# Kernel tuning notes

Measured on AMD Instinct MI355X. Metric: run time of the kernel, lower is better.

The kernel has to match this reference:

```python
import jax, jax.numpy as jnp
import numpy as np

EPS_NORM = 1e-8   # matches torch F.normalize default-ish eps used in cosine_dist
CLAMP_MIN = 1e-12
CLAMP_MAX = 1e12

def setup_inputs() -> dict:
    key = jax.random.key(0)
    k1, k2, k3 = jax.random.split(key, 3)
    N, D, C = 262144, 256, 64
    ref_emb = jax.random.normal(k1, (N, D), dtype=jnp.float32)
    ref_label = jax.random.randint(k2, (N,), 0, C)
    centers = jax.random.normal(k3, (C, D), dtype=jnp.float32)
    return {"ref_emb": ref_emb, "ref_label": ref_label, "centers": centers}

def reference(ref_emb, ref_label, centers):
    # center[i] = centers[ref_label[i]]  -> [N, D] gather
    center = centers[ref_label]
    # diag of pairwise cosine-distance matrix == row-wise cosine distance
    # cos_dist_i = 1 - <x_i, c_i> / (||x_i|| * ||c_i||)
    dot = jnp.sum(ref_emb * center, axis=-1)                     # [N]
    nx = jnp.sqrt(jnp.sum(ref_emb * ref_emb, axis=-1))           # [N]
    nc = jnp.sqrt(jnp.sum(center * center, axis=-1))             # [N]
    cos_sim = dot / jnp.maximum(nx * nc, EPS_NORM)
    cos_diag = 1.0 - cos_sim
    return jnp.mean(jnp.clip(cos_diag, CLAMP_MIN, CLAMP_MAX), axis=-1)
```

## Files before the change

### kernel.cpp

```cpp
#include <hip/hip_runtime.h>
#include <math.h>

constexpr int N = 262144;
constexpr int D = 256;
constexpr int C = 64;
constexpr float CLAMP_MIN = 1e-12f;
constexpr float CLAMP_MAX = 1e12f;

constexpr int BLOCKS = 2048;
constexpr int NWAVES = BLOCKS * 4;
constexpr int GPW    = (N / 4) / NWAVES;

__global__ __launch_bounds__(64) void center_normalize_kernel(
        const float* __restrict__ centers, float* __restrict__ cn) {
    const int c = blockIdx.x;
    const int lane = threadIdx.x;
    float4 v = reinterpret_cast<const float4*>(centers + c * D)[lane];
    float s = v.x * v.x + v.y * v.y + v.z * v.z + v.w * v.w;
    #pragma unroll
    for (int off = 32; off >= 1; off >>= 1)
        s += __shfl_xor(s, off, 64);
    const float inv = rsqrtf(fmaxf(s, 1e-24f));
    float4 o = make_float4(v.x * inv, v.y * inv, v.z * inv, v.w * inv);
    reinterpret_cast<float4*>(cn + c * D)[lane] = o;
}

__global__ __launch_bounds__(256) void inner_cos_kernel(
        const float* __restrict__ emb,
        const int*   __restrict__ label,
        const float* __restrict__ cnormed,
        float* __restrict__ partials) {
    const int lane = threadIdx.x & 63;
    const int wave = threadIdx.x >> 6;
    const int sub  = lane & 15;
    const int quad = lane >> 4;
    const int gwave = (blockIdx.x << 2) | wave;

    int mylab = 0;
    if (lane < 32) {
        const int k = lane >> 2, q = lane & 3;
        mylab = label[4 * gwave + k * (4 * NWAVES) + q];
    }

    const float4* xbase = reinterpret_cast<const float4*>(emb);
    const float4* cbase = reinterpret_cast<const float4*>(cnormed);

    float lsum = 0.0f;
    float4 x[4], c[4];

    {
        const int lab  = __shfl(mylab, quad);
        const int row0 = 4 * gwave + quad;
        const float4* xr = xbase + (size_t)row0 * (D / 4);
        const float4* cr = cbase + (size_t)lab  * (D / 4);
        #pragma unroll
        for (int j = 0; j < 4; ++j) { x[j] = xr[(j << 4) + sub]; c[j] = cr[(j << 4) + sub]; }
    }

    #pragma unroll
    for (int k = 0; k < GPW; ++k) {
        float4 xn[4], cn[4];
        if (k + 1 < GPW) {
            const int labn = __shfl(mylab, ((k + 1) << 2) + quad);
            const int rown = 4 * gwave + (k + 1) * (4 * NWAVES) + quad;
            const float4* xr = xbase + (size_t)rown * (D / 4);
            const float4* cr = cbase + (size_t)labn * (D / 4);
            #pragma unroll
            for (int j = 0; j < 4; ++j) { xn[j] = xr[(j << 4) + sub]; cn[j] = cr[(j << 4) + sub]; }
        }

        float dot = 0.0f, nx2 = 0.0f;
        #pragma unroll
        for (int j = 0; j < 4; ++j) {
            dot = fmaf(x[j].x, c[j].x, dot); dot = fmaf(x[j].y, c[j].y, dot);
            dot = fmaf(x[j].z, c[j].z, dot); dot = fmaf(x[j].w, c[j].w, dot);
            nx2 = fmaf(x[j].x, x[j].x, nx2); nx2 = fmaf(x[j].y, x[j].y, nx2);
            nx2 = fmaf(x[j].z, x[j].z, nx2); nx2 = fmaf(x[j].w, x[j].w, nx2);
        }
        #pragma unroll
        for (int off = 8; off >= 1; off >>= 1) {
            dot += __shfl_xor(dot, off, 64);
            nx2 += __shfl_xor(nx2, off, 64);
        }
        float cd = 1.0f - dot * rsqrtf(fmaxf(nx2, 1e-24f));
        cd = fminf(fmaxf(cd, CLAMP_MIN), CLAMP_MAX);
        lsum += cd;

        if (k + 1 < GPW) {
            #pragma unroll
            for (int j = 0; j < 4; ++j) { x[j] = xn[j]; c[j] = cn[j]; }
        }
    }

    lsum += __shfl_xor(lsum, 16, 64);
    lsum += __shfl_xor(lsum, 32, 64);

    __shared__ float ssum[4];
    if (lane == 0) ssum[wave] = lsum;
    __syncthreads();
    if (threadIdx.x == 0)
        partials[blockIdx.x] = (ssum[0] + ssum[1]) + (ssum[2] + ssum[3]);
}

__global__ __launch_bounds__(256) void finalize_kernel(
        const float* __restrict__ partials, float* __restrict__ out) {
    float s = 0.0f;
    #pragma unroll
    for (int i = 0; i < BLOCKS / 256; ++i)
        s += partials[threadIdx.x + (i << 8)];
    #pragma unroll
    for (int off = 32; off >= 1; off >>= 1)
        s += __shfl_xor(s, off, 64);
    __shared__ float ss[4];
    if ((threadIdx.x & 63) == 0) ss[threadIdx.x >> 6] = s;
    __syncthreads();
    if (threadIdx.x == 0)
        out[0] = ((ss[0] + ss[1]) + (ss[2] + ss[3])) * (1.0f / (float)N);
}

extern "C" void kernel_launch(void* const* d_in, const int* in_sizes, int n_in,
                              void* d_out, int out_size, void* d_ws, size_t ws_size,
                              hipStream_t stream) {
    const float* emb     = (const float*)d_in[0];
    const int*   label   = (const int*)d_in[1];
    const float* centers = (const float*)d_in[2];
    float* out      = (float*)d_out;
    float* cnormed  = (float*)d_ws;
    float* partials = (float*)d_ws + C * D;

    center_normalize_kernel<<<C, 64, 0, stream>>>(centers, cnormed);
    inner_cos_kernel<<<BLOCKS, 256, 0, stream>>>(emb, label, cnormed, partials);
    finalize_kernel<<<1, 256, 0, stream>>>(partials, out);
}
```

Before: 357.4 us.

## Stage normalized centers in LDS and use nontemporal embedding loads

Each 1024-thread block copies the whole normalized center table into shared memory, and center rows are then read from LDS instead of being gathered from global memory. Embedding rows are loaded with nontemporal hints, and the grid changes to 512 blocks of 16 waves. This is meant to remove redundant global and L2 traffic for center gathers and keep the streamed embeddings from polluting the cache. The cost is a 64 KB per-block LDS fill, a block-wide barrier before compute, and lower occupancy.

```diff
diff --git a/kernel.cpp b/kernel.cpp
--- a/kernel.cpp
+++ b/kernel.cpp
@@ -7,9 +7,12 @@
 constexpr float CLAMP_MIN = 1e-12f;
 constexpr float CLAMP_MAX = 1e12f;
 
-constexpr int BLOCKS = 2048;
-constexpr int NWAVES = BLOCKS * 4;
-constexpr int GPW    = (N / 4) / NWAVES;
+constexpr int BLOCKS  = 512;
+constexpr int WPB     = 16;
+constexpr int NWAVES  = BLOCKS * WPB;
+constexpr int GPW     = (N / 4) / NWAVES;
+
+typedef float fvec4 __attribute__((ext_vector_type(4)));
 
 __global__ __launch_bounds__(64) void center_normalize_kernel(
         const float* __restrict__ centers, float* __restrict__ cn) {
@@ -25,16 +28,26 @@
     reinterpret_cast<float4*>(cn + c * D)[lane] = o;
 }
 
-__global__ __launch_bounds__(256) void inner_cos_kernel(
+__global__ __launch_bounds__(1024) void inner_cos_kernel(
         const float* __restrict__ emb,
         const int*   __restrict__ label,
         const float* __restrict__ cnormed,
         float* __restrict__ partials) {
+    __shared__ float4 ctab[C * D / 4];
+    __shared__ float  ssum[WPB];
+
+    {
+        const float4* src = reinterpret_cast<const float4*>(cnormed);
+        #pragma unroll
+        for (int i = 0; i < (C * D / 4) / 1024; ++i)
+            ctab[threadIdx.x + i * 1024] = src[threadIdx.x + i * 1024];
+    }
+
     const int lane = threadIdx.x & 63;
     const int wave = threadIdx.x >> 6;
     const int sub  = lane & 15;
     const int quad = lane >> 4;
-    const int gwave = (blockIdx.x << 2) | wave;
+    const int gwave = blockIdx.x * WPB + wave;
 
     int mylab = 0;
     if (lane < 32) {
@@ -42,38 +55,47 @@
         mylab = label[4 * gwave + k * (4 * NWAVES) + q];
     }
 
-    const float4* xbase = reinterpret_cast<const float4*>(emb);
-    const float4* cbase = reinterpret_cast<const float4*>(cnormed);
+    __syncthreads();
+
+    const fvec4* xbase = reinterpret_cast<const fvec4*>(emb);
 
     float lsum = 0.0f;
-    float4 x[4], c[4];
+    fvec4 x[4];
 
     {
-        const int lab  = __shfl(mylab, quad);
-        const int row0 = 4 * gwave + quad;
-        const float4* xr = xbase + (size_t)row0 * (D / 4);
-        const float4* cr = cbase + (size_t)lab  * (D / 4);
+        const fvec4* xr = xbase + (size_t)(4 * gwave + quad) * (D / 4);
         #pragma unroll
-        for (int j = 0; j < 4; ++j) { x[j] = xr[(j << 4) + sub]; c[j] = cr[(j << 4) + sub]; }
+        for (int j = 0; j < 4; ++j)
+            x[j] = __builtin_nontemporal_load(xr + (j << 4) + sub);
     }
 
     #pragma unroll
     for (int k = 0; k < GPW; ++k) {
-        float4 xn[4], cn[4];
+        fvec4 xn[4];
         if (k + 1 < GPW) {
-            const int labn = __shfl(mylab, ((k + 1) << 2) + quad);
             const int rown = 4 * gwave + (k + 1) * (4 * NWAVES) + quad;
-            const float4* xr = xbase + (size_t)rown * (D / 4);
-            const float4* cr = cbase + (size_t)labn * (D / 4);
+            const fvec4* xr = xbase + (size_t)rown * (D / 4);
             #pragma unroll
-            for (int j = 0; j < 4; ++j) { xn[j] = xr[(j << 4) + sub]; cn[j] = cr[(j << 4) + sub]; }
+            for (int j = 0; j < 4; ++j)
+                xn[j] = __builtin_nontemporal_load(xr + (j << 4) + sub);
         }
 
+        const int lab = __shfl(mylab, (k << 2) + quad);
+        const float4* crow = ctab + lab * (D / 4);
+        float4 c0 = crow[sub +  0], c1 = crow[sub + 16];
+        float4 c2 = crow[sub + 32], c3 = crow[sub + 48];
+
         float dot = 0.0f, nx2 = 0.0f;
+        dot = fmaf(x[0].x, c0.x, dot); dot = fmaf(x[0].y, c0.y, dot);
+        dot = fmaf(x[0].z, c0.z, dot); dot = fmaf(x[0].w, c0.w, dot);
+        dot = fmaf(x[1].x, c1.x, dot); dot = fmaf(x[1].y, c1.y, dot);
+        dot = fmaf(x[1].z, c1.z, dot); dot = fmaf(x[1].w, c1.w, dot);
+        dot = fmaf(x[2].x, c2.x, dot); dot = fmaf(x[2].y, c2.y, dot);
+        dot = fmaf(x[2].z, c2.z, dot); dot = fmaf(x[2].w, c2.w, dot);
+        dot = fmaf(x[3].x, c3.x, dot); dot = fmaf(x[3].y, c3.y, dot);
+        dot = fmaf(x[3].z, c3.z, dot); dot = fmaf(x[3].w, c3.w, dot);
         #pragma unroll
         for (int j = 0; j < 4; ++j) {
-            dot = fmaf(x[j].x, c[j].x, dot); dot = fmaf(x[j].y, c[j].y, dot);
-            dot = fmaf(x[j].z, c[j].z, dot); dot = fmaf(x[j].w, c[j].w, dot);
             nx2 = fmaf(x[j].x, x[j].x, nx2); nx2 = fmaf(x[j].y, x[j].y, nx2);
             nx2 = fmaf(x[j].z, x[j].z, nx2); nx2 = fmaf(x[j].w, x[j].w, nx2);
         }
@@ -88,18 +110,21 @@
 
         if (k + 1 < GPW) {
             #pragma unroll
-            for (int j = 0; j < 4; ++j) { x[j] = xn[j]; c[j] = cn[j]; }
+            for (int j = 0; j < 4; ++j) x[j] = xn[j];
         }
     }
 
     lsum += __shfl_xor(lsum, 16, 64);
     lsum += __shfl_xor(lsum, 32, 64);
 
-    __shared__ float ssum[4];
     if (lane == 0) ssum[wave] = lsum;
     __syncthreads();
-    if (threadIdx.x == 0)
-        partials[blockIdx.x] = (ssum[0] + ssum[1]) + (ssum[2] + ssum[3]);
+    if (threadIdx.x == 0) {
+        float s = 0.0f;
+        #pragma unroll
+        for (int w = 0; w < WPB; ++w) s += ssum[w];
+        partials[blockIdx.x] = s;
+    }
 }
 
 __global__ __launch_bounds__(256) void finalize_kernel(
@@ -129,6 +154,6 @@
     float* partials = (float*)d_ws + C * D;
 
     center_normalize_kernel<<<C, 64, 0, stream>>>(centers, cnormed);
-    inner_cos_kernel<<<BLOCKS, 256, 0, stream>>>(emb, label, cnormed, partials);
+    inner_cos_kernel<<<BLOCKS, 1024, 0, stream>>>(emb, label, cnormed, partials);
     finalize_kernel<<<1, 256, 0, stream>>>(partials, out);
 }
```

After: 334.8 us. -6.3%, faster.
